# Performance work log

Measured on AMD Instinct MI355X. Metric: run time of the kernel, lower is better.

The kernel has to match this reference:

```python
import jax, jax.numpy as jnp
import numpy as np

HEAD_DIM = 32
KS = 3        # kernel_size
DIL = 2       # dilation
SCALE = HEAD_DIM ** -0.5


def _unfold_1d(x, ks, dil):
    """Emulate nn.Unfold(ks, dil, dil*(ks-1)//2, 1) applied to x[:, :, :, None].

    x: [B, d, N]. The input is treated as an N x 1 image, so of the ks*ks
    window slots only the center width-column gathers real values; the rest
    are zero padding (faithful to the torch module).
    Returns [B, d, ks*ks, N].
    """
    B, d, N = x.shape
    pad = dil * (ks - 1) // 2
    xp = jnp.pad(x, ((0, 0), (0, 0), (pad, pad)))
    # shifted rows along the sequence (height) axis: [B, d, ks, N]
    rows = jnp.stack([xp[:, :, i * dil:i * dil + N] for i in range(ks)], axis=2)
    c = (ks - 1) // 2
    full = jnp.zeros((B, d, ks, ks, N), x.dtype).at[:, :, :, c, :].set(rows)
    return full.reshape(B, d, ks * ks, N)


def setup_inputs() -> dict:
    key = jax.random.key(0)
    kq, kk, kv = jax.random.split(key, 3)
    B, d, N = 4, 256, 8192
    return {
        "q": jax.random.normal(kq, (B, d, N), dtype=jnp.float32),
        "k": jax.random.normal(kk, (B, d, N), dtype=jnp.float32),
        "v": jax.random.normal(kv, (B, d, N), dtype=jnp.float32),
    }


def reference(q, k, v):
    B, d, N = q.shape
    h = d // HEAD_DIM
    K = KS * KS
    qh = q.reshape(B, h, HEAD_DIM, N)                       # [B,h,hd,N]
    kw = _unfold_1d(k, KS, DIL).reshape(B, h, HEAD_DIM, K, N)
    vw = _unfold_1d(v, KS, DIL).reshape(B, h, HEAD_DIM, K, N)
    attn = jnp.einsum('bhdn,bhdkn->bhnk', qh, kw) * SCALE    # [B,h,N,K]
    attn = jax.nn.softmax(attn, axis=-1)
    x = jnp.einsum('bhnk,bhdkn->bhnd', attn, vw)             # [B,h,N,hd]
    return x.transpose(0, 2, 1, 3).reshape(B, N, d)
```

## Files before the change

### kernel.cpp

```cpp
#include <hip/hip_runtime.h>


constexpr int Bn = 4;
constexpr int Dd = 256;
constexpr int Nn = 8192;
constexpr int HD = 32;
constexpr int Hh = Dd / HD;
constexpr float SCALE = 0.17677669529663687f;

typedef float vfloat4 __attribute__((ext_vector_type(4)));

__global__ __launch_bounds__(256) void dilate_attn_kernel(
    const float* __restrict__ q,
    const float* __restrict__ k,
    const float* __restrict__ v,
    float* __restrict__ out)
{
    const int tid  = threadIdx.x;
    const int lane = tid & 63;
    const int subq = lane & 7;
    const int cg   = lane >> 3;
    const int w    = tid >> 6;

    const int blk  = blockIdx.x;
    const int bh   = blk >> 6;
    const int h    = bh & (Hh - 1);
    const int b    = bh >> 3;
    const int n0 = ((blk & 63) << 7) + (w << 5) + (subq << 2);

    const int cb = (b * Dd + h * HD + cg * 4) * Nn + n0;
    const float* qb = q + cb;
    const float* kb = k + cb;
    const float* vb = v + cb;

    const bool hasL = (n0 >= 4);
    const bool hasR = (n0 + 4 < Nn);

    float s0[4] = {0.f, 0.f, 0.f, 0.f};
    float s1[4] = {0.f, 0.f, 0.f, 0.f};
    float s2[4] = {0.f, 0.f, 0.f, 0.f};
    #pragma unroll
    for (int c = 0; c < 4; ++c) {
        const int o = c * Nn;
        const float4 qc = *reinterpret_cast<const float4*>(qb + o);
        const float4 kc = *reinterpret_cast<const float4*>(kb + o);
        float2 km = make_float2(0.f, 0.f), kp = make_float2(0.f, 0.f);
        if (hasL) km = *reinterpret_cast<const float2*>(kb + o - 2);
        if (hasR) kp = *reinterpret_cast<const float2*>(kb + o + 4);
        s0[0] = fmaf(qc.x, km.x, s0[0]);
        s1[0] = fmaf(qc.x, kc.x, s1[0]);
        s2[0] = fmaf(qc.x, kc.z, s2[0]);
        s0[1] = fmaf(qc.y, km.y, s0[1]);
        s1[1] = fmaf(qc.y, kc.y, s1[1]);
        s2[1] = fmaf(qc.y, kc.w, s2[1]);
        s0[2] = fmaf(qc.z, kc.x, s0[2]);
        s1[2] = fmaf(qc.z, kc.z, s1[2]);
        s2[2] = fmaf(qc.z, kp.x, s2[2]);
        s0[3] = fmaf(qc.w, kc.y, s0[3]);
        s1[3] = fmaf(qc.w, kc.w, s1[3]);
        s2[3] = fmaf(qc.w, kp.y, s2[3]);
    }

    float p0[4], p1[4], p2[4];
    #pragma unroll
    for (int j = 0; j < 4; ++j) {
        float a = s0[j], bb = s1[j], cc = s2[j];
        a  += __shfl_xor(a,  8, 64); a  += __shfl_xor(a, 16, 64); a  += __shfl_xor(a, 32, 64);
        bb += __shfl_xor(bb, 8, 64); bb += __shfl_xor(bb, 16, 64); bb += __shfl_xor(bb, 32, 64);
        cc += __shfl_xor(cc, 8, 64); cc += __shfl_xor(cc, 16, 64); cc += __shfl_xor(cc, 32, 64);
        a *= SCALE; bb *= SCALE; cc *= SCALE;
        const float m  = fmaxf(fmaxf(a, bb), fmaxf(cc, 0.f));
        const float e0 = __expf(a - m);
        const float e1 = __expf(bb - m);
        const float e2 = __expf(cc - m);
        const float inv = 1.f / (e0 + e1 + e2 + 6.f * __expf(-m));
        p0[j] = e0 * inv; p1[j] = e1 * inv; p2[j] = e2 * inv;
    }

    float t[4][4];
    #pragma unroll
    for (int c = 0; c < 4; ++c) {
        const int o = c * Nn;
        const float4 vc = *reinterpret_cast<const float4*>(vb + o);
        float2 vm = make_float2(0.f, 0.f), vp = make_float2(0.f, 0.f);
        if (hasL) vm = *reinterpret_cast<const float2*>(vb + o - 2);
        if (hasR) vp = *reinterpret_cast<const float2*>(vb + o + 4);
        t[0][c] = fmaf(p0[0], vm.x, fmaf(p1[0], vc.x, p2[0] * vc.z));
        t[1][c] = fmaf(p0[1], vm.y, fmaf(p1[1], vc.y, p2[1] * vc.w));
        t[2][c] = fmaf(p0[2], vc.x, fmaf(p1[2], vc.z, p2[2] * vp.x));
        t[3][c] = fmaf(p0[3], vc.y, fmaf(p1[3], vc.w, p2[3] * vp.y));
    }

    float* ob = out + (b * Nn + n0) * Dd + h * HD + cg * 4;
    #pragma unroll
    for (int j = 0; j < 4; ++j) {
        vfloat4 a = {t[j][0], t[j][1], t[j][2], t[j][3]};
        __builtin_nontemporal_store(a, reinterpret_cast<vfloat4*>(ob + j * Dd));
    }
}

extern "C" void kernel_launch(void* const* d_in, const int* in_sizes, int n_in,
                              void* d_out, int out_size, void* d_ws, size_t ws_size,
                              hipStream_t stream)
{
    const float* q = (const float*)d_in[0];
    const float* k = (const float*)d_in[1];
    const float* v = (const float*)d_in[2];
    float* out = (float*)d_out;

    const int total_threads = Bn * Hh * (Nn / 4) * 8;
    dilate_attn_kernel<<<total_threads / 256, 256, 0, stream>>>(q, k, v, out);
}
```

Measured before the change: 29.64 us.

## Process two position groups per thread, issue all loads upfront, swizzle block order

Each thread now handles two 4-position groups 128 apart, so the grid is halved. All q, k and v loads for both groups are issued before any compute, which raises memory-level parallelism and lets v loads overlap the softmax. Block indices are remapped so that consecutive blocks are spread across batch-head slices, presumably to spread traffic across XCDs and memory channels. The cost is higher register pressure and fewer blocks in flight.

New measurement: 27.24 us. 1.09x faster.

```diff
diff --git a/kernel.cpp b/kernel.cpp
--- a/kernel.cpp
+++ b/kernel.cpp
@@ -22,80 +22,112 @@
     const int cg   = lane >> 3;
     const int w    = tid >> 6;
 
-    const int blk  = blockIdx.x;
-    const int bh   = blk >> 6;
+    const int orig = ((blockIdx.x & 7) << 7) + (blockIdx.x >> 3);
+    const int bh   = orig >> 5;
     const int h    = bh & (Hh - 1);
     const int b    = bh >> 3;
-    const int n0 = ((blk & 63) << 7) + (w << 5) + (subq << 2);
+    const int nbase = ((orig & 31) << 8) + (w << 5) + (subq << 2);
 
-    const int cb = (b * Dd + h * HD + cg * 4) * Nn + n0;
-    const float* qb = q + cb;
-    const float* kb = k + cb;
-    const float* vb = v + cb;
+    int   n0[2];  n0[0] = nbase;  n0[1] = nbase + 128;
+    const int cbase = (b * Dd + h * HD + cg * 4) * Nn;
 
-    const bool hasL = (n0 >= 4);
-    const bool hasR = (n0 + 4 < Nn);
-
-    float s0[4] = {0.f, 0.f, 0.f, 0.f};
-    float s1[4] = {0.f, 0.f, 0.f, 0.f};
-    float s2[4] = {0.f, 0.f, 0.f, 0.f};
+    const float* qb[2];  const float* kb[2];  const float* vb[2];
+    bool hasL[2], hasR[2];
     #pragma unroll
-    for (int c = 0; c < 4; ++c) {
-        const int o = c * Nn;
-        const float4 qc = *reinterpret_cast<const float4*>(qb + o);
-        const float4 kc = *reinterpret_cast<const float4*>(kb + o);
-        float2 km = make_float2(0.f, 0.f), kp = make_float2(0.f, 0.f);
-        if (hasL) km = *reinterpret_cast<const float2*>(kb + o - 2);
-        if (hasR) kp = *reinterpret_cast<const float2*>(kb + o + 4);
-        s0[0] = fmaf(qc.x, km.x, s0[0]);
-        s1[0] = fmaf(qc.x, kc.x, s1[0]);
-        s2[0] = fmaf(qc.x, kc.z, s2[0]);
-        s0[1] = fmaf(qc.y, km.y, s0[1]);
-        s1[1] = fmaf(qc.y, kc.y, s1[1]);
-        s2[1] = fmaf(qc.y, kc.w, s2[1]);
-        s0[2] = fmaf(qc.z, kc.x, s0[2]);
-        s1[2] = fmaf(qc.z, kc.z, s1[2]);
-        s2[2] = fmaf(qc.z, kp.x, s2[2]);
-        s0[3] = fmaf(qc.w, kc.y, s0[3]);
-        s1[3] = fmaf(qc.w, kc.w, s1[3]);
-        s2[3] = fmaf(qc.w, kp.y, s2[3]);
+    for (int u = 0; u < 2; ++u) {
+        qb[u] = q + cbase + n0[u];
+        kb[u] = k + cbase + n0[u];
+        vb[u] = v + cbase + n0[u];
+        hasL[u] = (n0[u] >= 4);
+        hasR[u] = (n0[u] + 4 < Nn);
     }
 
-    float p0[4], p1[4], p2[4];
+    float4 qv[2][4], kc4[2][4], vc4[2][4];
+    float2 km2[2][4], kp2[2][4], vm2[2][4], vp2[2][4];
     #pragma unroll
-    for (int j = 0; j < 4; ++j) {
-        float a = s0[j], bb = s1[j], cc = s2[j];
-        a  += __shfl_xor(a,  8, 64); a  += __shfl_xor(a, 16, 64); a  += __shfl_xor(a, 32, 64);
-        bb += __shfl_xor(bb, 8, 64); bb += __shfl_xor(bb, 16, 64); bb += __shfl_xor(bb, 32, 64);
-        cc += __shfl_xor(cc, 8, 64); cc += __shfl_xor(cc, 16, 64); cc += __shfl_xor(cc, 32, 64);
-        a *= SCALE; bb *= SCALE; cc *= SCALE;
-        const float m  = fmaxf(fmaxf(a, bb), fmaxf(cc, 0.f));
-        const float e0 = __expf(a - m);
-        const float e1 = __expf(bb - m);
-        const float e2 = __expf(cc - m);
-        const float inv = 1.f / (e0 + e1 + e2 + 6.f * __expf(-m));
-        p0[j] = e0 * inv; p1[j] = e1 * inv; p2[j] = e2 * inv;
+    for (int u = 0; u < 2; ++u) {
+        #pragma unroll
+        for (int c = 0; c < 4; ++c) {
+            const int o = c * Nn;
+            qv[u][c]  = *reinterpret_cast<const float4*>(qb[u] + o);
+            kc4[u][c] = *reinterpret_cast<const float4*>(kb[u] + o);
+            km2[u][c] = hasL[u] ? *reinterpret_cast<const float2*>(kb[u] + o - 2) : make_float2(0.f, 0.f);
+            kp2[u][c] = hasR[u] ? *reinterpret_cast<const float2*>(kb[u] + o + 4) : make_float2(0.f, 0.f);
+        }
+    }
+    #pragma unroll
+    for (int u = 0; u < 2; ++u) {
+        #pragma unroll
+        for (int c = 0; c < 4; ++c) {
+            const int o = c * Nn;
+            vc4[u][c] = *reinterpret_cast<const float4*>(vb[u] + o);
+            vm2[u][c] = hasL[u] ? *reinterpret_cast<const float2*>(vb[u] + o - 2) : make_float2(0.f, 0.f);
+            vp2[u][c] = hasR[u] ? *reinterpret_cast<const float2*>(vb[u] + o + 4) : make_float2(0.f, 0.f);
+        }
     }
 
-    float t[4][4];
+    float s0[2][4] = {}, s1[2][4] = {}, s2[2][4] = {};
     #pragma unroll
-    for (int c = 0; c < 4; ++c) {
-        const int o = c * Nn;
-        const float4 vc = *reinterpret_cast<const float4*>(vb + o);
-        float2 vm = make_float2(0.f, 0.f), vp = make_float2(0.f, 0.f);
-        if (hasL) vm = *reinterpret_cast<const float2*>(vb + o - 2);
-        if (hasR) vp = *reinterpret_cast<const float2*>(vb + o + 4);
-        t[0][c] = fmaf(p0[0], vm.x, fmaf(p1[0], vc.x, p2[0] * vc.z));
-        t[1][c] = fmaf(p0[1], vm.y, fmaf(p1[1], vc.y, p2[1] * vc.w));
-        t[2][c] = fmaf(p0[2], vc.x, fmaf(p1[2], vc.z, p2[2] * vp.x));
-        t[3][c] = fmaf(p0[3], vc.y, fmaf(p1[3], vc.w, p2[3] * vp.y));
+    for (int u = 0; u < 2; ++u) {
+        #pragma unroll
+        for (int c = 0; c < 4; ++c) {
+            const float4 qc = qv[u][c];
+            const float4 kc = kc4[u][c];
+            const float2 km = km2[u][c];
+            const float2 kp = kp2[u][c];
+            s0[u][0] = fmaf(qc.x, km.x, s0[u][0]);
+            s1[u][0] = fmaf(qc.x, kc.x, s1[u][0]);
+            s2[u][0] = fmaf(qc.x, kc.z, s2[u][0]);
+            s0[u][1] = fmaf(qc.y, km.y, s0[u][1]);
+            s1[u][1] = fmaf(qc.y, kc.y, s1[u][1]);
+            s2[u][1] = fmaf(qc.y, kc.w, s2[u][1]);
+            s0[u][2] = fmaf(qc.z, kc.x, s0[u][2]);
+            s1[u][2] = fmaf(qc.z, kc.z, s1[u][2]);
+            s2[u][2] = fmaf(qc.z, kp.x, s2[u][2]);
+            s0[u][3] = fmaf(qc.w, kc.y, s0[u][3]);
+            s1[u][3] = fmaf(qc.w, kc.w, s1[u][3]);
+            s2[u][3] = fmaf(qc.w, kp.y, s2[u][3]);
+        }
     }
 
-    float* ob = out + (b * Nn + n0) * Dd + h * HD + cg * 4;
+    float p0[2][4], p1[2][4], p2[2][4];
     #pragma unroll
-    for (int j = 0; j < 4; ++j) {
-        vfloat4 a = {t[j][0], t[j][1], t[j][2], t[j][3]};
-        __builtin_nontemporal_store(a, reinterpret_cast<vfloat4*>(ob + j * Dd));
+    for (int u = 0; u < 2; ++u) {
+        #pragma unroll
+        for (int j = 0; j < 4; ++j) {
+            float a = s0[u][j], bb = s1[u][j], cc = s2[u][j];
+            a  += __shfl_xor(a,  8, 64); a  += __shfl_xor(a, 16, 64); a  += __shfl_xor(a, 32, 64);
+            bb += __shfl_xor(bb, 8, 64); bb += __shfl_xor(bb, 16, 64); bb += __shfl_xor(bb, 32, 64);
+            cc += __shfl_xor(cc, 8, 64); cc += __shfl_xor(cc, 16, 64); cc += __shfl_xor(cc, 32, 64);
+            a *= SCALE; bb *= SCALE; cc *= SCALE;
+            const float m  = fmaxf(fmaxf(a, bb), fmaxf(cc, 0.f));
+            const float e0 = __expf(a - m);
+            const float e1 = __expf(bb - m);
+            const float e2 = __expf(cc - m);
+            const float inv = 1.f / (e0 + e1 + e2 + 6.f * __expf(-m));
+            p0[u][j] = e0 * inv; p1[u][j] = e1 * inv; p2[u][j] = e2 * inv;
+        }
+    }
+
+    #pragma unroll
+    for (int u = 0; u < 2; ++u) {
+        float t[4][4];
+        #pragma unroll
+        for (int c = 0; c < 4; ++c) {
+            const float4 vc = vc4[u][c];
+            const float2 vm = vm2[u][c];
+            const float2 vp = vp2[u][c];
+            t[0][c] = fmaf(p0[u][0], vm.x, fmaf(p1[u][0], vc.x, p2[u][0] * vc.z));
+            t[1][c] = fmaf(p0[u][1], vm.y, fmaf(p1[u][1], vc.y, p2[u][1] * vc.w));
+            t[2][c] = fmaf(p0[u][2], vc.x, fmaf(p1[u][2], vc.z, p2[u][2] * vp.x));
+            t[3][c] = fmaf(p0[u][3], vc.y, fmaf(p1[u][3], vc.w, p2[u][3] * vp.y));
+        }
+        float* ob = out + (b * Nn + n0[u]) * Dd + h * HD + cg * 4;
+        #pragma unroll
+        for (int j = 0; j < 4; ++j) {
+            vfloat4 a = {t[j][0], t[j][1], t[j][2], t[j][3]};
+            __builtin_nontemporal_store(a, reinterpret_cast<vfloat4*>(ob + j * Dd));
+        }
     }
 }
 
@@ -108,6 +140,6 @@
     const float* v = (const float*)d_in[2];
     float* out = (float*)d_out;
 
-    const int total_threads = Bn * Hh * (Nn / 4) * 8;
+    const int total_threads = Bn * Hh * (Nn / 8) * 8;
     dilate_attn_kernel<<<total_threads / 256, 256, 0, stream>>>(q, k, v, out);
 }
```

## Process four tiles per block with double-buffered register prefetch and block swizzle

Applied to the files above, without the earlier changes.

Each block now handles four consecutive 128-column tiles instead of one. The next tile's q/k/v loads are issued into a second register buffer before the current tile is computed, so memory latency overlaps with compute. The grid shrinks to 512 blocks with an XCD-style block index swizzle, and output stores drop the nontemporal hint. Risks are higher register pressure, fewer waves in flight to hide latency, and different cache behaviour for the stores.

Measured after the change: 29.47 us. No clear change (-0.6%).

```diff
diff --git a/kernel.cpp b/kernel.cpp
--- a/kernel.cpp
+++ b/kernel.cpp
@@ -10,43 +10,40 @@
 
 typedef float vfloat4 __attribute__((ext_vector_type(4)));
 
-__global__ __launch_bounds__(256) void dilate_attn_kernel(
-    const float* __restrict__ q,
-    const float* __restrict__ k,
-    const float* __restrict__ v,
-    float* __restrict__ out)
+struct Tile {
+    float4 qv[4], kc[4], vc[4];
+    float2 km[4], kp[4], vm[4], vp[4];
+};
+
+__device__ __forceinline__ void load_tile(Tile& T,
+    const float* __restrict__ q, const float* __restrict__ k,
+    const float* __restrict__ v, int cb, bool hasL, bool hasR)
 {
-    const int tid  = threadIdx.x;
-    const int lane = tid & 63;
-    const int subq = lane & 7;
-    const int cg   = lane >> 3;
-    const int w    = tid >> 6;
+    #pragma unroll
+    for (int c = 0; c < 4; ++c) {
+        const int o = c * Nn;
+        T.qv[c] = *reinterpret_cast<const float4*>(q + cb + o);
+        T.kc[c] = *reinterpret_cast<const float4*>(k + cb + o);
+        T.vc[c] = *reinterpret_cast<const float4*>(v + cb + o);
+        T.km[c] = hasL ? *reinterpret_cast<const float2*>(k + cb + o - 2) : make_float2(0.f, 0.f);
+        T.kp[c] = hasR ? *reinterpret_cast<const float2*>(k + cb + o + 4) : make_float2(0.f, 0.f);
+        T.vm[c] = hasL ? *reinterpret_cast<const float2*>(v + cb + o - 2) : make_float2(0.f, 0.f);
+        T.vp[c] = hasR ? *reinterpret_cast<const float2*>(v + cb + o + 4) : make_float2(0.f, 0.f);
+    }
+}
 
-    const int blk  = blockIdx.x;
-    const int bh   = blk >> 6;
-    const int h    = bh & (Hh - 1);
-    const int b    = bh >> 3;
-    const int n0 = ((blk & 63) << 7) + (w << 5) + (subq << 2);
-
-    const int cb = (b * Dd + h * HD + cg * 4) * Nn + n0;
-    const float* qb = q + cb;
-    const float* kb = k + cb;
-    const float* vb = v + cb;
-
-    const bool hasL = (n0 >= 4);
-    const bool hasR = (n0 + 4 < Nn);
-
+__device__ __forceinline__ void compute_store(const Tile& T,
+    float* __restrict__ out, int b, int n0, int h, int cg)
+{
     float s0[4] = {0.f, 0.f, 0.f, 0.f};
     float s1[4] = {0.f, 0.f, 0.f, 0.f};
     float s2[4] = {0.f, 0.f, 0.f, 0.f};
     #pragma unroll
     for (int c = 0; c < 4; ++c) {
-        const int o = c * Nn;
-        const float4 qc = *reinterpret_cast<const float4*>(qb + o);
-        const float4 kc = *reinterpret_cast<const float4*>(kb + o);
-        float2 km = make_float2(0.f, 0.f), kp = make_float2(0.f, 0.f);
-        if (hasL) km = *reinterpret_cast<const float2*>(kb + o - 2);
-        if (hasR) kp = *reinterpret_cast<const float2*>(kb + o + 4);
+        const float4 qc = T.qv[c];
+        const float4 kc = T.kc[c];
+        const float2 km = T.km[c];
+        const float2 kp = T.kp[c];
         s0[0] = fmaf(qc.x, km.x, s0[0]);
         s1[0] = fmaf(qc.x, kc.x, s1[0]);
         s2[0] = fmaf(qc.x, kc.z, s2[0]);
@@ -80,11 +77,9 @@
     float t[4][4];
     #pragma unroll
     for (int c = 0; c < 4; ++c) {
-        const int o = c * Nn;
-        const float4 vc = *reinterpret_cast<const float4*>(vb + o);
-        float2 vm = make_float2(0.f, 0.f), vp = make_float2(0.f, 0.f);
-        if (hasL) vm = *reinterpret_cast<const float2*>(vb + o - 2);
-        if (hasR) vp = *reinterpret_cast<const float2*>(vb + o + 4);
+        const float4 vc = T.vc[c];
+        const float2 vm = T.vm[c];
+        const float2 vp = T.vp[c];
         t[0][c] = fmaf(p0[0], vm.x, fmaf(p1[0], vc.x, p2[0] * vc.z));
         t[1][c] = fmaf(p0[1], vm.y, fmaf(p1[1], vc.y, p2[1] * vc.w));
         t[2][c] = fmaf(p0[2], vc.x, fmaf(p1[2], vc.z, p2[2] * vp.x));
@@ -95,8 +90,44 @@
     #pragma unroll
     for (int j = 0; j < 4; ++j) {
         vfloat4 a = {t[j][0], t[j][1], t[j][2], t[j][3]};
-        __builtin_nontemporal_store(a, reinterpret_cast<vfloat4*>(ob + j * Dd));
+        *reinterpret_cast<vfloat4*>(ob + j * Dd) = a;
     }
+}
+
+__global__ __launch_bounds__(256) void dilate_attn_kernel(
+    const float* __restrict__ q,
+    const float* __restrict__ k,
+    const float* __restrict__ v,
+    float* __restrict__ out)
+{
+    const int tid  = threadIdx.x;
+    const int lane = tid & 63;
+    const int subq = lane & 7;
+    const int cg   = lane >> 3;
+    const int w    = tid >> 6;
+
+    const int orig = ((blockIdx.x & 7) << 6) + (blockIdx.x >> 3);
+    const int bh   = orig >> 4;
+    const int h    = bh & (Hh - 1);
+    const int b    = bh >> 3;
+    const int nt0 = ((orig & 15) << 9) + (w << 5) + (subq << 2);
+
+    const int cbase = (b * Dd + h * HD + cg * 4) * Nn;
+
+    Tile TA, TB;
+
+    load_tile(TA, q, k, v, cbase + nt0, nt0 >= 4, nt0 + 4 < Nn);
+
+    load_tile(TB, q, k, v, cbase + nt0 + 128, true, nt0 + 132 < Nn);
+    compute_store(TA, out, b, nt0, h, cg);
+
+    load_tile(TA, q, k, v, cbase + nt0 + 256, true, nt0 + 260 < Nn);
+    compute_store(TB, out, b, nt0 + 128, h, cg);
+
+    load_tile(TB, q, k, v, cbase + nt0 + 384, true, nt0 + 388 < Nn);
+    compute_store(TA, out, b, nt0 + 256, h, cg);
+
+    compute_store(TB, out, b, nt0 + 384, h, cg);
 }
 
 extern "C" void kernel_launch(void* const* d_in, const int* in_sizes, int n_in,
@@ -108,6 +139,5 @@
     const float* v = (const float*)d_in[2];
     float* out = (float*)d_out;
 
-    const int total_threads = Bn * Hh * (Nn / 4) * 8;
-    dilate_attn_kernel<<<total_threads / 256, 256, 0, stream>>>(q, k, v, out);
+    dilate_attn_kernel<<<512, 256, 0, stream>>>(q, k, v, out);
 }
```
